# Performance work log

Measured on AMD Instinct MI355X. Metric: run time of the kernel, lower is better.

Reference implementation:

```python
import jax, jax.numpy as jnp
import numpy as np

EPS = 1e-5

def setup_inputs() -> dict:
    key = jax.random.key(0)
    ks = jax.random.split(key, 10)
    B, N, D = 1, 20000, 256
    E, H = 320000, 8
    s = 1.0 / np.sqrt(D)
    return {
        "node_embeddings": jax.random.normal(ks[0], (B, N, D), jnp.float32),
        "edge_index": jax.random.randint(ks[1], (2, E), 0, N, jnp.int32),
        "edge_weights": jax.random.uniform(ks[2], (E,), jnp.float32),
        "Wq": jax.random.normal(ks[3], (D, D), jnp.float32) * s,
        "Wk": jax.random.normal(ks[4], (D, D), jnp.float32) * s,
        "Wv": jax.random.normal(ks[5], (D, D), jnp.float32) * s,
        "We": jax.random.normal(ks[6], (H,), jnp.float32),  # edge_encoder weight [num_heads,1] squeezed
        "Wo": jax.random.normal(ks[7], (D, D), jnp.float32) * s,
        "ln_g": jnp.ones((D,), jnp.float32),
        "ln_b": jnp.zeros((D,), jnp.float32),
    }

def reference(node_embeddings, edge_index, edge_weights, Wq, Wk, Wv, We, Wo, ln_g, ln_b):
    B, N, D = node_embeddings.shape
    H = We.shape[0]
    hd = D // H
    scale = 1.0 / np.sqrt(hd)
    residual = node_embeddings

    # projections -> [B, N, H, hd]
    Q = (node_embeddings @ Wq).reshape(B, N, H, hd)
    K = (node_embeddings @ Wk).reshape(B, N, H, hd)
    V = (node_embeddings @ Wv).reshape(B, N, H, hd)

    src = edge_index[0]
    tgt = edge_index[1]
    E = src.shape[0]

    # gather per edge, edge axis leading for segment ops: [E, B, H, hd]
    Q_e = jnp.moveaxis(Q[:, src], 1, 0)
    K_e = jnp.moveaxis(K[:, tgt], 1, 0)
    V_e = jnp.moveaxis(V[:, tgt], 1, 0)

    # per-edge scores [E, B, H]
    scores = (Q_e * K_e).sum(-1) * scale
    bias = edge_weights[:, None] * We[None, :]            # [E, H]
    scores = scores + bias[:, None, :]

    # scatter softmax grouped by source node
    m = jax.ops.segment_max(scores, src, num_segments=N)   # [N, B, H]
    p = jnp.exp(scores - m[src])
    denom = jax.ops.segment_sum(p, src, num_segments=N)    # [N, B, H]
    attn = p / denom[src]                                   # [E, B, H]

    # scatter-add weighted V -> [N, B, H, hd]
    weighted = attn[..., None] * V_e
    agg = jax.ops.segment_sum(weighted.reshape(E, -1), src, num_segments=N)
    agg = agg.reshape(N, B, H, hd)

    attn_out = jnp.moveaxis(agg, 0, 1).reshape(B, N, D)     # [B, N, D]
    out = attn_out @ Wo

    x = out + residual
    mu = x.mean(-1, keepdims=True)
    var = ((x - mu) ** 2).mean(-1, keepdims=True)
    return (x - mu) / jnp.sqrt(var + EPS) * ln_g + ln_b
```

## Files before the change

kernel.cpp:

```cpp
#include <hip/hip_runtime.h>
#include <hip/hip_bf16.h>

typedef __attribute__((ext_vector_type(8))) short short8;
typedef __attribute__((ext_vector_type(4))) short short4_t;
typedef __attribute__((ext_vector_type(4))) float f32x4;

#define CH 64

__device__ __forceinline__ ushort f2b(float f) {
  __hip_bfloat16 h = __float2bfloat16(f);
  return *reinterpret_cast<ushort*>(&h);
}
__device__ __forceinline__ float b2f(ushort u) {
  return __uint_as_float(((unsigned)u) << 16);
}
__device__ __forceinline__ void wave_lds_sync() {
  asm volatile("s_waitcnt lgkmcnt(0)" ::: "memory");
  __builtin_amdgcn_wave_barrier();
}

__global__ __launch_bounds__(256) void pre_kernel(
    const float* __restrict__ X, ushort* __restrict__ Xb, int nX,
    const float* __restrict__ Wq, const float* __restrict__ Wk,
    const float* __restrict__ Wv, const float* __restrict__ Wo,
    ushort* __restrict__ Wt, int* __restrict__ counts, int N, int nxb) {
  __shared__ float L[32][33];
  int b = blockIdx.x;
  int t = threadIdx.x;
  if (b < nxb) {
    int i = (b * 256 + t) * 8;
    if (i >= nX) return;
    float4 x0 = *reinterpret_cast<const float4*>(X + i);
    float4 x1 = *reinterpret_cast<const float4*>(X + i + 4);
    short8 o;
    o[0] = (short)f2b(x0.x); o[1] = (short)f2b(x0.y);
    o[2] = (short)f2b(x0.z); o[3] = (short)f2b(x0.w);
    o[4] = (short)f2b(x1.x); o[5] = (short)f2b(x1.y);
    o[6] = (short)f2b(x1.z); o[7] = (short)f2b(x1.w);
    *reinterpret_cast<short8*>(Xb + i) = o;
  } else if (b < nxb + 256) {
    int bx = b - nxb;
    int mat = bx >> 6;
    int tile = bx & 63;
    int tr = (tile >> 3) * 32;
    int tc = (tile & 7) * 32;
    const float* W = (mat == 0) ? Wq : (mat == 1) ? Wk : (mat == 2) ? Wv : Wo;
    int c = t & 31, r8 = t >> 5;
#pragma unroll
    for (int rr = 0; rr < 4; ++rr) {
      int r = r8 + rr * 8;
      L[r][c] = W[(size_t)(tr + r) * 256 + tc + c];
    }
    __syncthreads();
#pragma unroll
    for (int rr = 0; rr < 4; ++rr) {
      int cc = r8 + rr * 8;
      Wt[(size_t)(mat * 256 + tc + cc) * 256 + tr + c] = f2b(L[c][cc]);
    }
  } else {
    int i = (b - nxb - 256) * 256 + t;
    if (i < N) counts[i] = 0;
  }
}

__global__ __launch_bounds__(256) void hist_gemm(
    const ushort* __restrict__ Xb, const ushort* __restrict__ Wt,
    ushort* __restrict__ QKVb, const int* __restrict__ src,
    int* __restrict__ counts, int N, int E, int ngemm) {
  __shared__ ushort sA[128 * 64];
  __shared__ ushort sB[128 * 64];
  int bid = blockIdx.x;
  int t = threadIdx.x;
  if (bid >= ngemm) {
    int e = (bid - ngemm) * 256 + t;
    if (e < E) atomicAdd(&counts[src[e]], 1);
    return;
  }
  int bx = bid / 6, by = bid % 6;
  char* cA = (char*)sA;
  char* cB = (char*)sB;
  int lane = t & 63, w = t >> 6;
  int wr = w >> 1, wc = w & 1;
  int row0 = bx * 128;
  int lr = lane & 15, kg = lane >> 4;
  f32x4 acc[4][4] = {};
  for (int k0 = 0; k0 < 256; k0 += 64) {
#pragma unroll
    for (int it = 0; it < 4; ++it) {
      int slot = t + it * 256;
      int row = slot >> 3, kc = slot & 7;
      int grow = min(row0 + row, N - 1);
      short8 va = *reinterpret_cast<const short8*>(Xb + (size_t)grow * 256 + k0 + kc * 8);
      *reinterpret_cast<short8*>(cA + ((row * 128 + kc * 16) ^ ((row & 7) << 4))) = va;
      short8 vb = *reinterpret_cast<const short8*>(Wt + (size_t)(by * 128 + row) * 256 + k0 + kc * 8);
      *reinterpret_cast<short8*>(cB + ((row * 128 + kc * 16) ^ ((row & 7) << 4))) = vb;
    }
    __syncthreads();
#pragma unroll
    for (int ks = 0; ks < 2; ++ks) {
      short8 af[4], bf[4];
#pragma unroll
      for (int fr = 0; fr < 4; ++fr) {
        int row = wr * 64 + fr * 16 + lr;
        af[fr] = *reinterpret_cast<const short8*>(
            cA + ((row * 128 + ks * 64 + kg * 16) ^ ((row & 7) << 4)));
      }
#pragma unroll
      for (int fc = 0; fc < 4; ++fc) {
        int col = wc * 64 + fc * 16 + lr;
        bf[fc] = *reinterpret_cast<const short8*>(
            cB + ((col * 128 + ks * 64 + kg * 16) ^ ((col & 7) << 4)));
      }
#pragma unroll
      for (int fr = 0; fr < 4; ++fr)
#pragma unroll
        for (int fc = 0; fc < 4; ++fc)
          acc[fr][fc] = __builtin_amdgcn_mfma_f32_16x16x32_bf16(af[fr], bf[fc], acc[fr][fc], 0, 0, 0);
    }
    __syncthreads();
  }
  int orow = kg * 4;
#pragma unroll
  for (int fr = 0; fr < 4; ++fr)
#pragma unroll
    for (int fc = 0; fc < 4; ++fc)
#pragma unroll
      for (int r = 0; r < 4; ++r) {
        int row = row0 + wr * 64 + fr * 16 + orow + r;
        int col = by * 128 + wc * 64 + fc * 16 + lr;
        if (row < N) QKVb[(size_t)row * 768 + col] = f2b(acc[fr][fc][r]);
      }
}

__global__ __launch_bounds__(1024) void scan_kernel(
    const int* __restrict__ counts, int* __restrict__ offs, int* __restrict__ cursor, int N) {
  __shared__ int wexc[16];
  __shared__ int s_total;
  __shared__ int carry_s;
  int t = threadIdx.x;
  int lane = t & 63, wv = t >> 6;
  __shared__ int wsum[16];
  if (t == 0) carry_s = 0;
  __syncthreads();
  for (int base = 0; base < N; base += 1024) {
    int i = base + t;
    int v = (i < N) ? counts[i] : 0;
    int x = v;
#pragma unroll
    for (int off = 1; off < 64; off <<= 1) {
      int y = __shfl_up(x, off);
      if (lane >= off) x += y;
    }
    if (lane == 63) wsum[wv] = x;
    __syncthreads();
    if (t < 64) {
      int s = (lane < 16) ? wsum[lane] : 0;
      int xs = s;
#pragma unroll
      for (int off = 1; off < 16; off <<= 1) {
        int y = __shfl_up(xs, off);
        if (lane >= off) xs += y;
      }
      if (lane < 16) wexc[lane] = xs - s;
      if (lane == 15) s_total = xs;
    }
    __syncthreads();
    int carry = carry_s;
    int excl = carry + wexc[wv] + (x - v);
    if (i < N) { offs[i] = excl; cursor[i] = excl; }
    __syncthreads();
    if (t == 0) carry_s += s_total;
    __syncthreads();
  }
  if (t == 0) offs[N] = carry_s;
}

__global__ void scatter_kernel(const int* __restrict__ src, const int* __restrict__ tgt,
                               const float* __restrict__ ew, int* __restrict__ cursor,
                               int* __restrict__ tgt_s, float* __restrict__ w_s, int E) {
  int e = blockIdx.x * blockDim.x + threadIdx.x;
  if (e < E) {
    int pos = atomicAdd(&cursor[src[e]], 1);
    tgt_s[pos] = tgt[e];
    w_s[pos] = ew[e];
  }
}

__global__ __launch_bounds__(256) void attn_kernel(
    const ushort* __restrict__ QKVb,
    const int* __restrict__ offs, const int* __restrict__ tgt_s, const float* __restrict__ w_s,
    const float* __restrict__ We, ushort* __restrict__ AGGb, int N) {
  __shared__ float s_p[4][CH][8];
  __shared__ int s_tgt[4][CH];
  __shared__ float s_w[4][CH];
  int t = threadIdx.x;
  int w = t >> 6;
  int l = t & 63;
  int i = blockIdx.x * 4 + w;
  if (i >= N) return;
  int e8 = l >> 3;
  int h = l & 7;
  int hacc = l >> 3;
  const float scale = 0.17677669529663687f;
  float we = We[h];

  float qf[32];
  {
    const short8* qr = reinterpret_cast<const short8*>(QKVb + (size_t)i * 768 + h * 32);
#pragma unroll
    for (int d = 0; d < 4; ++d) {
      short8 qv = qr[d];
#pragma unroll
      for (int x = 0; x < 8; ++x) qf[d * 8 + x] = b2f((ushort)qv[x]);
    }
  }

  float m = -1e30f, lsum = 0.f;
  float acc0 = 0.f, acc1 = 0.f, acc2 = 0.f, acc3 = 0.f;
  int beg = offs[i], end = offs[i + 1];

  for (int base = beg; base < end; base += CH) {
    int cnt = min(CH, end - base);
    int cnt_pad = (cnt + 7) & ~7;
    {
      bool valid = l < cnt;
      int tg = valid ? tgt_s[base + l] : i;
      float ww = valid ? w_s[base + l] : 0.f;
      s_tgt[w][l] = tg;
      s_w[w][l] = ww;
    }
    wave_lds_sync();

    float s_local[8];
#pragma unroll
    for (int it = 0; it < 8; ++it) s_local[it] = -1e30f;

    short8 kc[4], kn[4];
    {
      const short8* p = reinterpret_cast<const short8*>(
          QKVb + (size_t)s_tgt[w][e8] * 768 + 256 + h * 32);
#pragma unroll
      for (int d = 0; d < 4; ++d) kc[d] = p[d];
    }
    if (8 < cnt_pad) {
      const short8* p = reinterpret_cast<const short8*>(
          QKVb + (size_t)s_tgt[w][8 + e8] * 768 + 256 + h * 32);
#pragma unroll
      for (int d = 0; d < 4; ++d) kn[d] = p[d];
    }
    float cmax = -1e30f;
#pragma unroll
    for (int it = 0; it < 8; ++it) {
      if (it * 8 >= cnt_pad) break;
      float dot = 0.f;
#pragma unroll
      for (int d = 0; d < 4; ++d)
#pragma unroll
        for (int x = 0; x < 8; ++x)
          dot += qf[d * 8 + x] * b2f((ushort)kc[d][x]);
      int j = it * 8 + e8;
      float s = (j < cnt) ? dot * scale + s_w[w][j] * we : -1e30f;
      s_local[it] = s;
      cmax = fmaxf(cmax, s);
#pragma unroll
      for (int d = 0; d < 4; ++d) kc[d] = kn[d];
      if ((it + 2) * 8 < cnt_pad) {
        const short8* p = reinterpret_cast<const short8*>(
            QKVb + (size_t)s_tgt[w][(it + 2) * 8 + e8] * 768 + 256 + h * 32);
#pragma unroll
        for (int d = 0; d < 4; ++d) kn[d] = p[d];
      }
    }
    cmax = fmaxf(cmax, __shfl_xor(cmax, 8));
    cmax = fmaxf(cmax, __shfl_xor(cmax, 16));
    cmax = fmaxf(cmax, __shfl_xor(cmax, 32));
    float newm = fmaxf(m, cmax);
    float f = __expf(m - newm);
    float psum = 0.f;
#pragma unroll
    for (int it = 0; it < 8; ++it) {
      if (it * 8 >= cnt_pad) break;
      int j = it * 8 + e8;
      float p = __expf(s_local[it] - newm);
      s_p[w][j][h] = p;
      psum += p;
    }
    psum += __shfl_xor(psum, 8);
    psum += __shfl_xor(psum, 16);
    psum += __shfl_xor(psum, 32);
    lsum = lsum * f + psum;
    m = newm;
    float f_acc = __shfl(f, hacc);
    acc0 *= f_acc; acc1 *= f_acc; acc2 *= f_acc; acc3 *= f_acc;
    wave_lds_sync();

#pragma unroll
    for (int g = 0; g < 8; ++g) {
      if (g * 8 >= cnt_pad) break;
      float pv[8];
      short4_t vv[8];
#pragma unroll
      for (int k = 0; k < 8; ++k) {
        int j = g * 8 + k;
        pv[k] = s_p[w][j][hacc];
        vv[k] = *reinterpret_cast<const short4_t*>(
            QKVb + (size_t)s_tgt[w][j] * 768 + 512 + l * 4);
      }
#pragma unroll
      for (int k = 0; k < 8; ++k) {
        acc0 += pv[k] * b2f((ushort)vv[k][0]);
        acc1 += pv[k] * b2f((ushort)vv[k][1]);
        acc2 += pv[k] * b2f((ushort)vv[k][2]);
        acc3 += pv[k] * b2f((ushort)vv[k][3]);
      }
    }
    wave_lds_sync();
  }
  float lsum_acc = __shfl(lsum, hacc);
  float rinv = (lsum_acc > 0.f) ? 1.f / lsum_acc : 0.f;
  short4_t o;
  o[0] = (short)f2b(acc0 * rinv);
  o[1] = (short)f2b(acc1 * rinv);
  o[2] = (short)f2b(acc2 * rinv);
  o[3] = (short)f2b(acc3 * rinv);
  *reinterpret_cast<short4_t*>(AGGb + (size_t)i * 256 + l * 4) = o;
}

__global__ __launch_bounds__(256) void out_ln(
    const ushort* __restrict__ AGGb, const ushort* __restrict__ Wot,
    const float* __restrict__ X, const float* __restrict__ g, const float* __restrict__ bb,
    float* __restrict__ out, int N) {
  __shared__ ushort sA[64 * 64];
  __shared__ ushort sB[256 * 64];
  char* cA = (char*)sA;
  char* cB = (char*)sB;
  int t = threadIdx.x;
  int lane = t & 63, w = t >> 6;
  int row0 = blockIdx.x * 64;
  int lr = lane & 15, kg = lane >> 4;
  f32x4 acc[16] = {};
  for (int k0 = 0; k0 < 256; k0 += 64) {
#pragma unroll
    for (int it = 0; it < 2; ++it) {
      int slot = t + it * 256;
      int row = slot >> 3, kc = slot & 7;
      int grow = min(row0 + row, N - 1);
      short8 va = *reinterpret_cast<const short8*>(AGGb + (size_t)grow * 256 + k0 + kc * 8);
      *reinterpret_cast<short8*>(cA + ((row * 128 + kc * 16) ^ ((row & 7) << 4))) = va;
    }
#pragma unroll
    for (int it = 0; it < 8; ++it) {
      int slot = t + it * 256;
      int col = slot >> 3, kc = slot & 7;
      short8 vb = *reinterpret_cast<const short8*>(Wot + (size_t)col * 256 + k0 + kc * 8);
      *reinterpret_cast<short8*>(cB + ((col * 128 + kc * 16) ^ ((col & 7) << 4))) = vb;
    }
    __syncthreads();
#pragma unroll
    for (int ks = 0; ks < 2; ++ks) {
      int arow = w * 16 + lr;
      short8 a = *reinterpret_cast<const short8*>(
          cA + ((arow * 128 + ks * 64 + kg * 16) ^ ((arow & 7) << 4)));
#pragma unroll
      for (int fc = 0; fc < 16; ++fc) {
        int col = fc * 16 + lr;
        short8 b = *reinterpret_cast<const short8*>(
            cB + ((col * 128 + ks * 64 + kg * 16) ^ ((col & 7) << 4)));
        acc[fc] = __builtin_amdgcn_mfma_f32_16x16x32_bf16(a, b, acc[fc], 0, 0, 0);
      }
    }
    __syncthreads();
  }
  float g16[16], b16[16];
#pragma unroll
  for (int fc = 0; fc < 16; ++fc) {
    g16[fc] = g[fc * 16 + lr];
    b16[fc] = bb[fc * 16 + lr];
  }
#pragma unroll
  for (int r = 0; r < 4; ++r) {
    int rowl = kg * 4 + r;
    int grow = row0 + w * 16 + rowl;
    int growc = min(grow, N - 1);
    float xv[16];
    float s = 0.f, ss = 0.f;
#pragma unroll
    for (int fc = 0; fc < 16; ++fc) {
      float v = acc[fc][r] + X[(size_t)growc * 256 + fc * 16 + lr];
      xv[fc] = v;
      s += v;
      ss += v * v;
    }
    s += __shfl_xor(s, 1);  ss += __shfl_xor(ss, 1);
    s += __shfl_xor(s, 2);  ss += __shfl_xor(ss, 2);
    s += __shfl_xor(s, 4);  ss += __shfl_xor(ss, 4);
    s += __shfl_xor(s, 8);  ss += __shfl_xor(ss, 8);
    float mu = s * (1.f / 256.f);
    float var = ss * (1.f / 256.f) - mu * mu;
    float rs = rsqrtf(var + 1e-5f);
    if (grow < N) {
#pragma unroll
      for (int fc = 0; fc < 16; ++fc)
        out[(size_t)grow * 256 + fc * 16 + lr] = (xv[fc] - mu) * rs * g16[fc] + b16[fc];
    }
  }
}

extern "C" void kernel_launch(void* const* d_in, const int* in_sizes, int n_in,
                              void* d_out, int out_size, void* d_ws, size_t ws_size,
                              hipStream_t stream) {
  const float* X  = (const float*)d_in[0];
  const int* eidx = (const int*)d_in[1];
  const float* ew = (const float*)d_in[2];
  const float* Wq = (const float*)d_in[3];
  const float* Wk = (const float*)d_in[4];
  const float* Wv = (const float*)d_in[5];
  const float* We = (const float*)d_in[6];
  const float* Wo = (const float*)d_in[7];
  const float* g  = (const float*)d_in[8];
  const float* b  = (const float*)d_in[9];
  int N = in_sizes[0] / 256;
  int E = in_sizes[1] / 2;
  const int* src = eidx;
  const int* tgt = eidx + E;
  float* out = (float*)d_out;

  char* w = (char*)d_ws;
  ushort* Xb   = (ushort*)w;  w += (size_t)N * 256 * 2;
  ushort* Wt   = (ushort*)w;  w += (size_t)1024 * 256 * 2;
  ushort* QKVb = (ushort*)w;  w += (size_t)N * 768 * 2;
  ushort* AGGb = (ushort*)w;  w += (size_t)N * 256 * 2;
  int* counts  = (int*)w;     w += (size_t)N * 4;
  int* offs    = (int*)w;     w += (size_t)(N + 1) * 4;
  int* cursor  = (int*)w;     w += (size_t)N * 4;
  int* tgt_s   = (int*)w;     w += (size_t)E * 4;
  float* w_s   = (float*)w;   w += (size_t)E * 4;
  const ushort* Wot = Wt + (size_t)768 * 256;

  int nX = N * 256;
  int nxb = (nX / 8 + 255) / 256;
  int nzero = (N + 255) / 256;
  pre_kernel<<<nxb + 256 + nzero, 256, 0, stream>>>(X, Xb, nX, Wq, Wk, Wv, Wo, Wt, counts, N, nxb);

  int ngemm = ((N + 127) / 128) * 6;
  int nhist = (E + 255) / 256;
  hist_gemm<<<ngemm + nhist, 256, 0, stream>>>(Xb, Wt, QKVb, src, counts, N, E, ngemm);

  scan_kernel<<<1, 1024, 0, stream>>>(counts, offs, cursor, N);
  scatter_kernel<<<(E + 255) / 256, 256, 0, stream>>>(src, tgt, ew, cursor, tgt_s, w_s, E);
  attn_kernel<<<(N + 3) / 4, 256, 0, stream>>>(QKVb, offs, tgt_s, w_s, We, AGGb, N);
  out_ln<<<(N + 63) / 64, 256, 0, stream>>>(AGGb, Wot, X, g, b, out, N);
}
```

Baseline: 143.7 us.

## Prefetch V rows across score phase and parallelize scan over contiguous chunks

The attention kernel now issues the V-row gathers for the first two groups of 8 edges before computing scores. It then double-buffers later V groups during the weighted-sum loop, so gather latency overlaps with the score and softmax work. The scan kernel drops its serial 1024-element block loop with several barriers per iteration. Each thread now sums a contiguous chunk, one block-wide scan runs, and each thread writes its offsets sequentially. The cost is higher register pressure in the attention kernel from 16 extra short4 buffers, and uncoalesced strided access in the scan.

```diff
diff --git a/kernel.cpp b/kernel.cpp
--- a/kernel.cpp
+++ b/kernel.cpp
@@ -134,45 +134,44 @@
 
 __global__ __launch_bounds__(1024) void scan_kernel(
     const int* __restrict__ counts, int* __restrict__ offs, int* __restrict__ cursor, int N) {
+  __shared__ int wsum[16];
   __shared__ int wexc[16];
   __shared__ int s_total;
-  __shared__ int carry_s;
   int t = threadIdx.x;
   int lane = t & 63, wv = t >> 6;
-  __shared__ int wsum[16];
-  if (t == 0) carry_s = 0;
+  int per = (N + 1023) >> 10;
+  int b0 = t * per;
+  int e0 = min(b0 + per, N);
+  int sum = 0;
+  for (int i = b0; i < e0; ++i) sum += counts[i];
+  int x = sum;
+#pragma unroll
+  for (int off = 1; off < 64; off <<= 1) {
+    int y = __shfl_up(x, off);
+    if (lane >= off) x += y;
+  }
+  if (lane == 63) wsum[wv] = x;
   __syncthreads();
-  for (int base = 0; base < N; base += 1024) {
-    int i = base + t;
-    int v = (i < N) ? counts[i] : 0;
-    int x = v;
-#pragma unroll
-    for (int off = 1; off < 64; off <<= 1) {
-      int y = __shfl_up(x, off);
-      if (lane >= off) x += y;
-    }
-    if (lane == 63) wsum[wv] = x;
-    __syncthreads();
-    if (t < 64) {
-      int s = (lane < 16) ? wsum[lane] : 0;
-      int xs = s;
-#pragma unroll
-      for (int off = 1; off < 16; off <<= 1) {
-        int y = __shfl_up(xs, off);
-        if (lane >= off) xs += y;
-      }
-      if (lane < 16) wexc[lane] = xs - s;
-      if (lane == 15) s_total = xs;
-    }
-    __syncthreads();
-    int carry = carry_s;
-    int excl = carry + wexc[wv] + (x - v);
-    if (i < N) { offs[i] = excl; cursor[i] = excl; }
-    __syncthreads();
-    if (t == 0) carry_s += s_total;
-    __syncthreads();
-  }
-  if (t == 0) offs[N] = carry_s;
+  if (t < 64) {
+    int s = (lane < 16) ? wsum[lane] : 0;
+    int xs = s;
+#pragma unroll
+    for (int off = 1; off < 16; off <<= 1) {
+      int y = __shfl_up(xs, off);
+      if (lane >= off) xs += y;
+    }
+    if (lane < 16) wexc[lane] = xs - s;
+    if (lane == 15) s_total = xs;
+  }
+  __syncthreads();
+  int running = wexc[wv] + (x - sum);
+  for (int i = b0; i < e0; ++i) {
+    int c = counts[i];
+    offs[i] = running;
+    cursor[i] = running;
+    running += c;
+  }
+  if (t == 0) offs[N] = s_total;
 }
 
 __global__ void scatter_kernel(const int* __restrict__ src, const int* __restrict__ tgt,
@@ -231,10 +230,6 @@
     }
     wave_lds_sync();
 
-    float s_local[8];
-#pragma unroll
-    for (int it = 0; it < 8; ++it) s_local[it] = -1e30f;
-
     short8 kc[4], kn[4];
     {
       const short8* p = reinterpret_cast<const short8*>(
@@ -248,6 +243,21 @@
 #pragma unroll
       for (int d = 0; d < 4; ++d) kn[d] = p[d];
     }
+    short4_t vc[8], vn[8];
+#pragma unroll
+    for (int k = 0; k < 8; ++k)
+      vc[k] = *reinterpret_cast<const short4_t*>(
+          QKVb + (size_t)s_tgt[w][k] * 768 + 512 + l * 4);
+    if (8 < cnt_pad) {
+#pragma unroll
+      for (int k = 0; k < 8; ++k)
+        vn[k] = *reinterpret_cast<const short4_t*>(
+            QKVb + (size_t)s_tgt[w][8 + k] * 768 + 512 + l * 4);
+    }
+
+    float s_local[8];
+#pragma unroll
+    for (int it = 0; it < 8; ++it) s_local[it] = -1e30f;
     float cmax = -1e30f;
 #pragma unroll
     for (int it = 0; it < 8; ++it) {
@@ -298,20 +308,22 @@
     for (int g = 0; g < 8; ++g) {
       if (g * 8 >= cnt_pad) break;
       float pv[8];
-      short4_t vv[8];
+#pragma unroll
+      for (int k = 0; k < 8; ++k) pv[k] = s_p[w][g * 8 + k][hacc];
 #pragma unroll
       for (int k = 0; k < 8; ++k) {
-        int j = g * 8 + k;
-        pv[k] = s_p[w][j][hacc];
-        vv[k] = *reinterpret_cast<const short4_t*>(
-            QKVb + (size_t)s_tgt[w][j] * 768 + 512 + l * 4);
-      }
-#pragma unroll
-      for (int k = 0; k < 8; ++k) {
-        acc0 += pv[k] * b2f((ushort)vv[k][0]);
-        acc1 += pv[k] * b2f((ushort)vv[k][1]);
-        acc2 += pv[k] * b2f((ushort)vv[k][2]);
-        acc3 += pv[k] * b2f((ushort)vv[k][3]);
+        acc0 += pv[k] * b2f((ushort)vc[k][0]);
+        acc1 += pv[k] * b2f((ushort)vc[k][1]);
+        acc2 += pv[k] * b2f((ushort)vc[k][2]);
+        acc3 += pv[k] * b2f((ushort)vc[k][3]);
+      }
+#pragma unroll
+      for (int k = 0; k < 8; ++k) vc[k] = vn[k];
+      if ((g + 2) * 8 < cnt_pad) {
+#pragma unroll
+        for (int k = 0; k < 8; ++k)
+          vn[k] = *reinterpret_cast<const short4_t*>(
+              QKVb + (size_t)s_tgt[w][(g + 2) * 8 + k] * 768 + 512 + l * 4);
       }
     }
     wave_lds_sync();
```

Result: slower. 167.1 us (+16.2%).
